# Kernel tuning notes

Hardware: AMD Instinct MI355X
Metric: run time of the kernel (lower is better)

## Reference

```python
import jax, jax.numpy as jnp
import numpy as np

B, IN, OUT = 32768, 1024, 1024

def setup_inputs() -> dict:
    key = jax.random.key(0)
    k1, k2, k3 = jax.random.split(key, 3)
    bound = float(np.sqrt(6.0 / (IN + OUT)))  # xavier_uniform gain=1
    x = jax.random.normal(k1, (B, IN), dtype=jnp.float32)
    weight = jax.random.uniform(k2, (OUT, IN), dtype=jnp.float32, minval=-bound, maxval=bound)
    gate = jnp.abs(jax.random.uniform(k3, (OUT, IN), dtype=jnp.float32, minval=-bound, maxval=bound))  # one_sided init
    bias = jnp.zeros((OUT,), dtype=jnp.float32)
    return {"x": x, "weight": weight, "gate": gate, "bias": bias}

def reference(x, weight, gate, bias):
    # in_bin = sign
    layer_in = jnp.sign(x)
    # drop_weights: weight * binarize_gate(gate) where binarize_gate = (sign(gate)+1)/2
    gate_mask = (jnp.sign(gate) + 1.0) * 0.5
    w = weight * gate_mask
    # weight_bin = sign (gated-off entries stay 0 since sign(0)=0)
    w = jnp.sign(w)
    # F.linear: x @ w.T + bias
    layer_out = jnp.einsum('bi,oi->bo', layer_in, w) + bias
    # adaptive scaling: abs-mean of raw input per row, abs-mean of raw weight per output
    in_scale = jnp.mean(jnp.abs(x), axis=1, keepdims=True)       # [B,1]
    weight_scale = jnp.mean(jnp.abs(weight), axis=1)             # [OUT]
    return in_scale * weight_scale * layer_out
```

## Files before the change

kernel.cpp:

```cpp
#include <hip/hip_runtime.h>

#define B_DIM 32768
#define IN_DIM 1024
#define OUT_DIM 1024

typedef int v4i __attribute__((ext_vector_type(4)));
typedef int v16i __attribute__((ext_vector_type(16)));

__device__ __forceinline__ int sgnb(float v) {
    return (v > 0.f) ? 1 : ((v < 0.f) ? 0xff : 0);
}

__device__ __forceinline__ int gsgnb(float w, float g) {
    return (g < 0.f) ? 0 : sgnb(w);
}

__global__ __launch_bounds__(256) void prep_kernel(
    const float* __restrict__ x, const float* __restrict__ w,
    const float* __restrict__ g,
    signed char* __restrict__ sx, signed char* __restrict__ wb,
    float* __restrict__ xscale, float* __restrict__ wscale) {
    const int wave = threadIdx.x >> 6;
    const int lane = threadIdx.x & 63;
    const int bq = blockIdx.x;
    if (bq < B_DIM / 4) {
        const int row = bq * 4 + wave;
        const float4* xr = (const float4*)(x + (size_t)row * IN_DIM);
        int* sr = (int*)(sx + (size_t)row * IN_DIM);
        float asum = 0.f;
#pragma unroll
        for (int it = 0; it < 4; ++it) {
            float4 v = xr[it * 64 + lane];
            asum += fabsf(v.x) + fabsf(v.y) + fabsf(v.z) + fabsf(v.w);
            sr[it * 64 + lane] =
                sgnb(v.x) | (sgnb(v.y) << 8) | (sgnb(v.z) << 16) | (sgnb(v.w) << 24);
        }
#pragma unroll
        for (int off = 32; off >= 1; off >>= 1) asum += __shfl_xor(asum, off, 64);
        if (lane == 0) xscale[row] = asum * (1.0f / IN_DIM);
    } else {
        const int row = (bq - B_DIM / 4) * 4 + wave;
        const float4* wr = (const float4*)(w + (size_t)row * IN_DIM);
        const float4* gr = (const float4*)(g + (size_t)row * IN_DIM);
        int* sr = (int*)(wb + (size_t)row * IN_DIM);
        float asum = 0.f;
#pragma unroll
        for (int it = 0; it < 4; ++it) {
            float4 wv = wr[it * 64 + lane];
            float4 gv = gr[it * 64 + lane];
            asum += fabsf(wv.x) + fabsf(wv.y) + fabsf(wv.z) + fabsf(wv.w);
            sr[it * 64 + lane] = gsgnb(wv.x, gv.x) | (gsgnb(wv.y, gv.y) << 8) |
                                 (gsgnb(wv.z, gv.z) << 16) | (gsgnb(wv.w, gv.w) << 24);
        }
#pragma unroll
        for (int off = 32; off >= 1; off >>= 1) asum += __shfl_xor(asum, off, 64);
        if (lane == 0) wscale[row] = asum * (1.0f / IN_DIM);
    }
}

__global__ __launch_bounds__(256) void gemm_i8_kernel(
    const signed char* __restrict__ A,
    const signed char* __restrict__ Bw,
    const float* __restrict__ xscale,
    const float* __restrict__ wscale,
    const float* __restrict__ bias,
    float* __restrict__ out) {
    __shared__ signed char smA[2][128 * 64];
    __shared__ signed char smB[2][128 * 64];

    const int t = threadIdx.x;
    const int wave = t >> 6, lane = t & 63;
    const int swz = (blockIdx.x & 7) * 256 + (blockIdx.x >> 3);
    const int bm = swz >> 3;
    const int bn = swz & 7;
    const int wr = wave >> 1, wc = wave & 1;

    const v16i vzero = {0, 0, 0, 0, 0, 0, 0, 0, 0, 0, 0, 0, 0, 0, 0, 0};
    v16i acc[2][2];
#pragma unroll
    for (int m = 0; m < 2; ++m)
#pragma unroll
        for (int n = 0; n < 2; ++n) acc[m][n] = vzero;

    const int r32 = lane & 31;
    const int kh = (lane >> 5) * 16;
    const size_t arow0 = (size_t)bm * 128;
    const size_t brow0 = (size_t)bn * 128;
    const int l_loff0 = wave * 1024;
    const int l_loff1 = 4096 + wave * 1024;
    const int srow0 = (l_loff0 + lane * 16) >> 6, scol0 = (l_loff0 + lane * 16) & 63;
    const int srow1 = (l_loff1 + lane * 16) >> 6, scol1 = (l_loff1 + lane * 16) & 63;

#define STAGE(BUF, K0)                                                          \
    do {                                                                        \
        __builtin_amdgcn_global_load_lds(                                       \
            (const __attribute__((address_space(1))) void*)(                    \
                A + (arow0 + srow0) * (size_t)IN_DIM + (K0) + scol0),           \
            (__attribute__((address_space(3))) void*)(smA[BUF] + l_loff0), 16, 0, 0); \
        __builtin_amdgcn_global_load_lds(                                       \
            (const __attribute__((address_space(1))) void*)(                    \
                Bw + (brow0 + srow0) * (size_t)IN_DIM + (K0) + scol0),          \
            (__attribute__((address_space(3))) void*)(smB[BUF] + l_loff0), 16, 0, 0); \
        __builtin_amdgcn_global_load_lds(                                       \
            (const __attribute__((address_space(1))) void*)(                    \
                A + (arow0 + srow1) * (size_t)IN_DIM + (K0) + scol1),           \
            (__attribute__((address_space(3))) void*)(smA[BUF] + l_loff1), 16, 0, 0); \
        __builtin_amdgcn_global_load_lds(                                       \
            (const __attribute__((address_space(1))) void*)(                    \
                Bw + (brow0 + srow1) * (size_t)IN_DIM + (K0) + scol1),          \
            (__attribute__((address_space(3))) void*)(smB[BUF] + l_loff1), 16, 0, 0); \
    } while (0)

#define COMPUTE(BUF)                                                            \
    do {                                                                        \
        _Pragma("unroll")                                                       \
        for (int ks = 0; ks < 2; ++ks) {                                        \
            v4i af[2], bf[2];                                                   \
            _Pragma("unroll")                                                   \
            for (int m = 0; m < 2; ++m)                                         \
                af[m] = *(const v4i*)(smA[BUF] +                                \
                        (wr * 64 + m * 32 + r32) * 64 + ks * 32 + kh);          \
            _Pragma("unroll")                                                   \
            for (int n = 0; n < 2; ++n)                                         \
                bf[n] = *(const v4i*)(smB[BUF] +                                \
                        (wc * 64 + n * 32 + r32) * 64 + ks * 32 + kh);          \
            _Pragma("unroll")                                                   \
            for (int m = 0; m < 2; ++m)                                         \
                _Pragma("unroll")                                               \
                for (int n = 0; n < 2; ++n)                                     \
                    acc[m][n] = __builtin_amdgcn_mfma_i32_32x32x32_i8(          \
                        af[m], bf[n], acc[m][n], 0, 0, 0);                      \
        }                                                                       \
    } while (0)

    STAGE(0, 0);
    __syncthreads();
#pragma unroll 1
    for (int kt = 0; kt < 7; ++kt) {
        STAGE(1, (2 * kt + 1) * 64);
        COMPUTE(0);
        __syncthreads();
        STAGE(0, (2 * kt + 2) * 64);
        COMPUTE(1);
        __syncthreads();
    }
    STAGE(1, 15 * 64);
    COMPUTE(0);
    __syncthreads();
    COMPUTE(1);
#undef STAGE
#undef COMPUTE

    const int col = lane & 31;
    const int rb = 4 * (lane >> 5);
    float wsc[2], bv[2];
    int gcolv[2];
#pragma unroll
    for (int n = 0; n < 2; ++n) {
        gcolv[n] = bn * 128 + wc * 64 + n * 32 + col;
        wsc[n] = wscale[gcolv[n]];
        bv[n] = bias[gcolv[n]];
    }
#pragma unroll
    for (int m = 0; m < 2; ++m) {
#pragma unroll
        for (int j = 0; j < 16; ++j) {
            const int grow = bm * 128 + wr * 64 + m * 32 + (j & 3) + 8 * (j >> 2) + rb;
            const float is = xscale[grow];
#pragma unroll
            for (int n = 0; n < 2; ++n) {
                out[(size_t)grow * OUT_DIM + gcolv[n]] =
                    is * wsc[n] * ((float)acc[m][n][j] + bv[n]);
            }
        }
    }
}

extern "C" void kernel_launch(void* const* d_in, const int* in_sizes, int n_in,
                              void* d_out, int out_size, void* d_ws, size_t ws_size,
                              hipStream_t stream) {
    const float* x = (const float*)d_in[0];
    const float* w = (const float*)d_in[1];
    const float* g = (const float*)d_in[2];
    const float* bias = (const float*)d_in[3];
    float* out = (float*)d_out;

    signed char* sx = (signed char*)d_ws;
    signed char* wb = sx + (size_t)B_DIM * IN_DIM;
    float* xscale = (float*)(wb + (size_t)OUT_DIM * IN_DIM);
    float* wscale = xscale + B_DIM;

    prep_kernel<<<B_DIM / 4 + OUT_DIM / 4, 256, 0, stream>>>(x, w, g, sx, wb,
                                                             xscale, wscale);
    gemm_i8_kernel<<<(B_DIM / 128) * (OUT_DIM / 128), 256, 0, stream>>>(
        sx, wb, xscale, wscale, bias, out);
}
```

Measured before the change: 276.6 us.

## Enlarge GEMM tile to 256x256 with 8 waves, swizzled LDS and finer pipeline

Grows the int8 GEMM block tile from 128x128 to 256x256 with 512 threads, so each wave computes 128x64 and gets more operand reuse per LDS read. Shared memory is split into k-halves of 32 bytes per row with an XOR swizzle to cut bank conflicts. The schedule moves to per-half phases with explicit s_barrier, s_waitcnt vmcnt and s_setprio around the MFMAs, so async global-to-LDS prefetch overlaps compute. This trades higher register and LDS use, and fewer blocks across the grid, for better reuse and overlap.

```diff
diff --git a/kernel.cpp b/kernel.cpp
--- a/kernel.cpp
+++ b/kernel.cpp
@@ -10,7 +10,6 @@
 __device__ __forceinline__ int sgnb(float v) {
     return (v > 0.f) ? 1 : ((v < 0.f) ? 0xff : 0);
 }
-
 __device__ __forceinline__ int gsgnb(float w, float g) {
     return (g < 0.f) ? 0 : sgnb(w);
 }
@@ -58,98 +57,104 @@
     }
 }
 
-__global__ __launch_bounds__(256) void gemm_i8_kernel(
+__global__ __launch_bounds__(512, 2) void gemm_i8_kernel(
     const signed char* __restrict__ A,
     const signed char* __restrict__ Bw,
     const float* __restrict__ xscale,
     const float* __restrict__ wscale,
     const float* __restrict__ bias,
     float* __restrict__ out) {
-    __shared__ signed char smA[2][128 * 64];
-    __shared__ signed char smB[2][128 * 64];
+    __shared__ signed char smA[2][16384];
+    __shared__ signed char smB[2][16384];
 
     const int t = threadIdx.x;
     const int wave = t >> 6, lane = t & 63;
-    const int swz = (blockIdx.x & 7) * 256 + (blockIdx.x >> 3);
-    const int bm = swz >> 3;
-    const int bn = swz & 7;
-    const int wr = wave >> 1, wc = wave & 1;
-
-    const v16i vzero = {0, 0, 0, 0, 0, 0, 0, 0, 0, 0, 0, 0, 0, 0, 0, 0};
-    v16i acc[2][2];
-#pragma unroll
-    for (int m = 0; m < 2; ++m)
-#pragma unroll
-        for (int n = 0; n < 2; ++n) acc[m][n] = vzero;
-
+    const int swz = (blockIdx.x & 7) * 64 + (blockIdx.x >> 3);
+    const int bm = swz >> 2;
+    const int bn = swz & 3;
+    const int wr = wave >> 2, wc = wave & 3;
     const int r32 = lane & 31;
-    const int kh = (lane >> 5) * 16;
-    const size_t arow0 = (size_t)bm * 128;
-    const size_t brow0 = (size_t)bn * 128;
-    const int l_loff0 = wave * 1024;
-    const int l_loff1 = 4096 + wave * 1024;
-    const int srow0 = (l_loff0 + lane * 16) >> 6, scol0 = (l_loff0 + lane * 16) & 63;
-    const int srow1 = (l_loff1 + lane * 16) >> 6, scol1 = (l_loff1 + lane * 16) & 63;
-
-#define STAGE(BUF, K0)                                                          \
-    do {                                                                        \
-        __builtin_amdgcn_global_load_lds(                                       \
-            (const __attribute__((address_space(1))) void*)(                    \
-                A + (arow0 + srow0) * (size_t)IN_DIM + (K0) + scol0),           \
-            (__attribute__((address_space(3))) void*)(smA[BUF] + l_loff0), 16, 0, 0); \
-        __builtin_amdgcn_global_load_lds(                                       \
-            (const __attribute__((address_space(1))) void*)(                    \
-                Bw + (brow0 + srow0) * (size_t)IN_DIM + (K0) + scol0),          \
-            (__attribute__((address_space(3))) void*)(smB[BUF] + l_loff0), 16, 0, 0); \
-        __builtin_amdgcn_global_load_lds(                                       \
-            (const __attribute__((address_space(1))) void*)(                    \
-                A + (arow0 + srow1) * (size_t)IN_DIM + (K0) + scol1),           \
-            (__attribute__((address_space(3))) void*)(smA[BUF] + l_loff1), 16, 0, 0); \
-        __builtin_amdgcn_global_load_lds(                                       \
-            (const __attribute__((address_space(1))) void*)(                    \
-                Bw + (brow0 + srow1) * (size_t)IN_DIM + (K0) + scol1),          \
-            (__attribute__((address_space(3))) void*)(smB[BUF] + l_loff1), 16, 0, 0); \
-    } while (0)
-
-#define COMPUTE(BUF)                                                            \
-    do {                                                                        \
-        _Pragma("unroll")                                                       \
-        for (int ks = 0; ks < 2; ++ks) {                                        \
-            v4i af[2], bf[2];                                                   \
-            _Pragma("unroll")                                                   \
-            for (int m = 0; m < 2; ++m)                                         \
-                af[m] = *(const v4i*)(smA[BUF] +                                \
-                        (wr * 64 + m * 32 + r32) * 64 + ks * 32 + kh);          \
-            _Pragma("unroll")                                                   \
-            for (int n = 0; n < 2; ++n)                                         \
-                bf[n] = *(const v4i*)(smB[BUF] +                                \
-                        (wc * 64 + n * 32 + r32) * 64 + ks * 32 + kh);          \
-            _Pragma("unroll")                                                   \
-            for (int m = 0; m < 2; ++m)                                         \
-                _Pragma("unroll")                                               \
-                for (int n = 0; n < 2; ++n)                                     \
-                    acc[m][n] = __builtin_amdgcn_mfma_i32_32x32x32_i8(          \
-                        af[m], bf[n], acc[m][n], 0, 0, 0);                      \
+    const int kh_eff = ((lane >> 5) << 4) ^ (((lane >> 2) & 1) << 4);
+
+    int aoff[4], boff[2];
+#pragma unroll
+    for (int m = 0; m < 4; ++m) aoff[m] = (wr * 128 + m * 32 + r32) * 32 + kh_eff;
+#pragma unroll
+    for (int n = 0; n < 2; ++n) boff[n] = (wc * 64 + n * 32 + r32) * 32 + kh_eff;
+
+    const int soff = wave * 1024 + lane * 16;
+    const int s_row = soff >> 5;
+    const int s_kh = (soff & 16) ^ (((s_row >> 2) & 1) << 4);
+    const size_t arow0 = (size_t)bm * 256;
+    const size_t brow0 = (size_t)bn * 256;
+    const signed char* aSrc = A + (((size_t)(arow0 + s_row)) << 10) + s_kh;
+    const signed char* bSrc = Bw + (((size_t)(brow0 + s_row)) << 10) + s_kh;
+
+    v16i acc[4][2];
+#pragma unroll
+    for (int m = 0; m < 4; ++m)
+#pragma unroll
+        for (int n = 0; n < 2; ++n)
+#pragma unroll
+            for (int j = 0; j < 16; ++j) acc[m][n][j] = 0;
+
+#define ISSUE_A(P, KS, K0)                                                      \
+    __builtin_amdgcn_global_load_lds(                                           \
+        (const __attribute__((address_space(1))) void*)(aSrc + (K0) + (KS)*32), \
+        (__attribute__((address_space(3))) void*)(&smA[P][(KS)*8192] + wave * 1024), \
+        16, 0, 0)
+#define ISSUE_B(P, KS, K0)                                                      \
+    __builtin_amdgcn_global_load_lds(                                           \
+        (const __attribute__((address_space(1))) void*)(bSrc + (K0) + (KS)*32), \
+        (__attribute__((address_space(3))) void*)(&smB[P][(KS)*8192] + wave * 1024), \
+        16, 0, 0)
+
+#define PHASE(P, KS, DOPREF, K0N, VMASM)                                        \
+    {                                                                           \
+        v4i af[4], bf[2];                                                       \
+        _Pragma("unroll") for (int m = 0; m < 4; ++m)                           \
+            af[m] = *(const v4i*)(&smA[P][(KS)*8192] + aoff[m]);                \
+        _Pragma("unroll") for (int n = 0; n < 2; ++n)                           \
+            bf[n] = *(const v4i*)(&smB[P][(KS)*8192] + boff[n]);                \
+        if (DOPREF) {                                                           \
+            ISSUE_A((P) ^ 1, KS, K0N);                                          \
+            ISSUE_B((P) ^ 1, KS, K0N);                                          \
         }                                                                       \
-    } while (0)
-
-    STAGE(0, 0);
-    __syncthreads();
+        __builtin_amdgcn_s_barrier();                                           \
+        __builtin_amdgcn_s_setprio(1);                                          \
+        _Pragma("unroll") for (int m = 0; m < 4; ++m) {                         \
+            acc[m][0] = __builtin_amdgcn_mfma_i32_32x32x32_i8(af[m], bf[0],     \
+                                                              acc[m][0], 0, 0, 0); \
+            acc[m][1] = __builtin_amdgcn_mfma_i32_32x32x32_i8(af[m], bf[1],     \
+                                                              acc[m][1], 0, 0, 0); \
+        }                                                                       \
+        __builtin_amdgcn_s_setprio(0);                                          \
+        VMASM;                                                                  \
+        __builtin_amdgcn_s_barrier();                                           \
+    }
+
+    ISSUE_A(0, 0, 0);
+    ISSUE_B(0, 0, 0);
+    ISSUE_A(0, 1, 0);
+    ISSUE_B(0, 1, 0);
+    asm volatile("s_waitcnt vmcnt(2)" ::: "memory");
+    __builtin_amdgcn_s_barrier();
+
 #pragma unroll 1
-    for (int kt = 0; kt < 7; ++kt) {
-        STAGE(1, (2 * kt + 1) * 64);
-        COMPUTE(0);
-        __syncthreads();
-        STAGE(0, (2 * kt + 2) * 64);
-        COMPUTE(1);
-        __syncthreads();
-    }
-    STAGE(1, 15 * 64);
-    COMPUTE(0);
-    __syncthreads();
-    COMPUTE(1);
-#undef STAGE
-#undef COMPUTE
+    for (int kt = 0; kt < 14; kt += 2) {
+        PHASE(0, 0, 1, (kt + 1) * 64, asm volatile("s_waitcnt vmcnt(2)" ::: "memory"));
+        PHASE(0, 1, 1, (kt + 1) * 64, asm volatile("s_waitcnt vmcnt(2)" ::: "memory"));
+        PHASE(1, 0, 1, (kt + 2) * 64, asm volatile("s_waitcnt vmcnt(2)" ::: "memory"));
+        PHASE(1, 1, 1, (kt + 2) * 64, asm volatile("s_waitcnt vmcnt(2)" ::: "memory"));
+    }
+    PHASE(0, 0, 1, 15 * 64, asm volatile("s_waitcnt vmcnt(2)" ::: "memory"));
+    PHASE(0, 1, 1, 15 * 64, asm volatile("s_waitcnt vmcnt(2)" ::: "memory"));
+    PHASE(1, 0, 0, 0, asm volatile("s_waitcnt vmcnt(0)" ::: "memory"));
+    PHASE(1, 1, 0, 0, (void)0);
+
+#undef PHASE
+#undef ISSUE_A
+#undef ISSUE_B
 
     const int col = lane & 31;
     const int rb = 4 * (lane >> 5);
@@ -157,15 +162,15 @@
     int gcolv[2];
 #pragma unroll
     for (int n = 0; n < 2; ++n) {
-        gcolv[n] = bn * 128 + wc * 64 + n * 32 + col;
+        gcolv[n] = bn * 256 + wc * 64 + n * 32 + col;
         wsc[n] = wscale[gcolv[n]];
         bv[n] = bias[gcolv[n]];
     }
 #pragma unroll
-    for (int m = 0; m < 2; ++m) {
+    for (int m = 0; m < 4; ++m) {
 #pragma unroll
         for (int j = 0; j < 16; ++j) {
-            const int grow = bm * 128 + wr * 64 + m * 32 + (j & 3) + 8 * (j >> 2) + rb;
+            const int grow = bm * 256 + wr * 128 + m * 32 + (j & 3) + 8 * (j >> 2) + rb;
             const float is = xscale[grow];
 #pragma unroll
             for (int n = 0; n < 2; ++n) {
@@ -192,6 +197,6 @@
 
     prep_kernel<<<B_DIM / 4 + OUT_DIM / 4, 256, 0, stream>>>(x, w, g, sx, wb,
                                                              xscale, wscale);
-    gemm_i8_kernel<<<(B_DIM / 128) * (OUT_DIM / 128), 256, 0, stream>>>(
+    gemm_i8_kernel<<<(B_DIM / 256) * (OUT_DIM / 256), 512, 0, stream>>>(
         sx, wb, xscale, wscale, bias, out);
 }
```

After: 288.3 us. 1.04x slower.
